# Optimization experiments

Measured on AMD Instinct MI355X. Metric: run time of the kernel, lower is better.

The kernel has to match this reference:

```python
import jax, jax.numpy as jnp
import numpy as np

TEMPERATURE = 0.2
NUMBER_CLASSES = 1000
LOSS_SCALE = 0.001

N, F = 8192, 256
M = 20000
DEPTH = 4


def setup_inputs() -> dict:
    key = jax.random.key(0)
    k1, k2, k3, k4 = jax.random.split(key, 4)
    gt_labels = jax.random.randint(k1, (N,), 0, NUMBER_CLASSES, dtype=jnp.int32)
    box_features = jax.random.normal(k2, (N, F), dtype=jnp.float32)
    memory = jax.random.normal(k3, (M, F), dtype=jnp.float32)
    trace_idx = jax.random.randint(k4, (NUMBER_CLASSES, DEPTH), 0, M, dtype=jnp.int32)
    return {"gt_labels": gt_labels, "box_features": box_features,
            "memory": memory, "trace_idx": trace_idx}


def reference(gt_labels, box_features, memory, trace_idx):
    # logits[i, j] = dot(f_i, m_j) / T  (the nested python loops fused into one GEMM)
    logits = jnp.einsum('nf,mf->nm', box_features, memory) / TEMPERATURE  # [N, M]
    # fenmu = sum_j exp(logits)  ->  log(fenmu) = logsumexp
    lse = jax.nn.logsumexp(logits, axis=-1)  # [N]
    # gather the trace entries for each item's label: [N, DEPTH]
    traces = trace_idx[gt_labels]  # [N, DEPTH]
    sel = jnp.take_along_axis(logits, traces, axis=1)  # [N, DEPTH]
    depth_w = jnp.arange(DEPTH, dtype=logits.dtype)  # gj = depth
    sum_gj = depth_w.sum()  # sum of layer weights (0+1+2+3)
    # per item: -sum_d gj * log(sim_d / fenmu) / sum_gj
    per_item = -jnp.sum((sel - lse[:, None]) * depth_w, axis=-1) / sum_gj  # [N]
    # background filter: items with label == number_classes contribute nothing
    fg = (gt_labels != NUMBER_CLASSES)
    loss = jnp.sum(jnp.where(fg, per_item, 0.0)) * LOSS_SCALE
    return loss
```

## Files before the change

### kernel.cpp

```cpp
#include <hip/hip_runtime.h>
#include <hip/hip_bf16.h>
#include <stdint.h>

#define NROWS 8192
#define FDIM 256
#define MCOLS 20000
#define NT32 625
#define MSPLIT 16
#define NCLS 1000
#define LOG2E 1.44269504088896f
#define LN2   0.69314718055994f


typedef short short8 __attribute__((ext_vector_type(8)));
typedef float f32x16 __attribute__((ext_vector_type(16)));

typedef __attribute__((address_space(3))) unsigned int lds_u32;
typedef const __attribute__((address_space(1))) unsigned int glb_u32;

__device__ __forceinline__ float ex2(float x) {
    float r;
    asm("v_exp_f32 %0, %1" : "=v"(r) : "v"(x));
    return r;
}

__device__ __forceinline__ unsigned short f2bf(float x) {
    unsigned u = __float_as_uint(x);
    unsigned r = (u + 0x7FFFu + ((u >> 16) & 1u)) >> 16;
    return (unsigned short)r;
}

__device__ __forceinline__ float vmax16(f32x16 v) {
    float x0 = fmaxf(fmaxf(v[0],  v[1]),  v[2]);
    float x1 = fmaxf(fmaxf(v[3],  v[4]),  v[5]);
    float x2 = fmaxf(fmaxf(v[6],  v[7]),  v[8]);
    float x3 = fmaxf(fmaxf(v[9],  v[10]), v[11]);
    float x4 = fmaxf(fmaxf(v[12], v[13]), v[14]);
    float x5 = fmaxf(fmaxf(x0, x1), x2);
    float x6 = fmaxf(fmaxf(x3, x4), v[15]);
    return fmaxf(x5, x6);
}

__global__ void conv_kernel(const float* __restrict__ in, unsigned short* __restrict__ out,
                            int n4, float scale) {
    int idx = blockIdx.x * blockDim.x + threadIdx.x;
    if (idx >= n4) return;
    float4 v = ((const float4*)in)[idx];
    ushort4 o;
    o.x = f2bf(v.x * scale); o.y = f2bf(v.y * scale);
    o.z = f2bf(v.z * scale); o.w = f2bf(v.w * scale);
    ((ushort4*)out)[idx] = o;
}

__global__ void conv_mb2(const float* __restrict__ in, unsigned short* __restrict__ out) {
    int g = blockIdx.x * 256 + threadIdx.x;
    int s = g & 63, kk = (g >> 6) & 15, t = g >> 10;
    const float* src = in + (size_t)(t * 32 + (s & 31)) * FDIM + kk * 16 + (s >> 5) * 8;
    float4 v0 = ((const float4*)src)[0];
    float4 v1 = ((const float4*)src)[1];
    short8 w;
    w[0] = (short)f2bf(v0.x); w[1] = (short)f2bf(v0.y);
    w[2] = (short)f2bf(v0.z); w[3] = (short)f2bf(v0.w);
    w[4] = (short)f2bf(v1.x); w[5] = (short)f2bf(v1.y);
    w[6] = (short)f2bf(v1.z); w[7] = (short)f2bf(v1.w);
    *(short8*)(out + (size_t)g * 8) = w;
}

__global__ void sel_kernel(const int* __restrict__ gt, const float* __restrict__ F,
                           const float* __restrict__ Mem, const int* __restrict__ trace,
                           float* __restrict__ wsel) {
    int lane = threadIdx.x & 63, wid = threadIdx.x >> 6;
    int i = blockIdx.x * 4 + wid;
    int label = gt[i];
    float w = 0.0f;
    if (label >= 0 && label < NCLS) {
        float4 fv = ((const float4*)(F + (size_t)i * FDIM))[lane];
        #pragma unroll
        for (int d = 1; d <= 3; ++d) {
            int tr = trace[label * 4 + d];
            float4 mv = ((const float4*)(Mem + (size_t)tr * FDIM))[lane];
            float dot = fv.x*mv.x + fv.y*mv.y + fv.z*mv.z + fv.w*mv.w;
            #pragma unroll
            for (int off = 32; off >= 1; off >>= 1) dot += __shfl_xor(dot, off, 64);
            w += (float)d * dot;
        }
    }
    if (lane == 0) wsel[i] = w * 5.0f;
}

__global__ __launch_bounds__(256, 2) void lse_gemm(
        const unsigned short* __restrict__ Fb, const unsigned short* __restrict__ Mb2,
        float* __restrict__ pm, float* __restrict__ ps) {
    __shared__ __align__(16) char smem[2 * 16384];

    const int split  = blockIdx.x;
    const int rowblk = blockIdx.y;
    const int tid  = threadIdx.x;
    const int lane = tid & 63, wid = tid >> 6;
    const int r0 = lane & 31;
    const int hi = lane >> 5;
    const int rowbase = rowblk * 256 + wid * 64;
    const int l16 = lane << 4;

    short8 al[16], ah[16];
    #pragma unroll
    for (int kk = 0; kk < 16; ++kk) {
        al[kk] = *(const short8*)(Fb + (size_t)(rowbase + r0)      * FDIM + kk * 16 + hi * 8);
        ah[kk] = *(const short8*)(Fb + (size_t)(rowbase + 32 + r0) * FDIM + kk * 16 + hi * 8);
    }

    float m0 = -3.0e38f, s0 = 0.0f, m1 = -3.0e38f, s1 = 0.0f;

    const int t0 = (split * NT32) / MSPLIT;
    const int t1 = ((split + 1) * NT32) / MSPLIT;

#define STAGE(BUF, t)                                                              \
    do {                                                                           \
        const char* srcT = (const char*)Mb2 + (size_t)(t) * 16384 + l16;           \
        _Pragma("unroll")                                                          \
        for (int c = 0; c < 4; ++c) {                                              \
            __builtin_amdgcn_global_load_lds(                                      \
                (glb_u32*)(srcT + (wid * 4 + c) * 1024),                           \
                (lds_u32*)(smem + (BUF) * 16384 + (wid * 4 + c) * 1024),           \
                16, 0, 0);                                                         \
        }                                                                          \
    } while (0)

#define BODYC(BUF)                                                                 \
    do {                                                                           \
        const char* bp = smem + (BUF) * 16384 + l16;                               \
        f32x16 accL = {0,0,0,0,0,0,0,0,0,0,0,0,0,0,0,0};                           \
        f32x16 accH = {0,0,0,0,0,0,0,0,0,0,0,0,0,0,0,0};                           \
        __builtin_amdgcn_s_setprio(1);                                             \
        _Pragma("unroll")                                                          \
        for (int kk = 0; kk < 16; ++kk) {                                          \
            short8 b = *(const short8*)(bp + kk * 1024);                           \
            accL = __builtin_amdgcn_mfma_f32_32x32x16_bf16(b, al[kk], accL, 0, 0, 0); \
            accH = __builtin_amdgcn_mfma_f32_32x32x16_bf16(b, ah[kk], accH, 0, 0, 0); \
        }                                                                          \
        __builtin_amdgcn_s_setprio(0);                                             \
        {                                                                          \
            float nm = fmaxf(vmax16(accL), m0);                                    \
            float p0 = 0.f, p1 = 0.f, p2 = 0.f, p3 = 0.f;                          \
            _Pragma("unroll")                                                      \
            for (int i = 0; i < 16; i += 4) {                                      \
                p0 += ex2(accL[i]     - nm); p1 += ex2(accL[i + 1] - nm);          \
                p2 += ex2(accL[i + 2] - nm); p3 += ex2(accL[i + 3] - nm);          \
            }                                                                      \
            s0 = fmaf(s0, ex2(m0 - nm), (p0 + p1) + (p2 + p3));                    \
            m0 = nm;                                                               \
        }                                                                          \
        {                                                                          \
            float nm = fmaxf(vmax16(accH), m1);                                    \
            float p0 = 0.f, p1 = 0.f, p2 = 0.f, p3 = 0.f;                          \
            _Pragma("unroll")                                                      \
            for (int i = 0; i < 16; i += 4) {                                      \
                p0 += ex2(accH[i]     - nm); p1 += ex2(accH[i + 1] - nm);          \
                p2 += ex2(accH[i + 2] - nm); p3 += ex2(accH[i + 3] - nm);          \
            }                                                                      \
            s1 = fmaf(s1, ex2(m1 - nm), (p0 + p1) + (p2 + p3));                    \
            m1 = nm;                                                               \
        }                                                                          \
    } while (0)

    STAGE(0, t0);
    __syncthreads();

    int t = t0;
    while (t + 2 <= t1) {
        STAGE(1, t + 1);
        BODYC(0);
        __syncthreads();
        if (t + 2 < t1) STAGE(0, t + 2);
        BODYC(1);
        __syncthreads();
        t += 2;
    }
    if (t < t1) BODYC(0);

#undef BODYC
#undef STAGE

    {
        float om = __shfl_xor(m0, 32, 64);
        float os = __shfl_xor(s0, 32, 64);
        float nm = fmaxf(m0, om);
        float sf = fmaf(s0, ex2(m0 - nm), os * ex2(om - nm));
        if (lane < 32) {
            pm[split * NROWS + rowbase + lane] = nm;
            ps[split * NROWS + rowbase + lane] = sf;
        }
    }
    {
        float om = __shfl_xor(m1, 32, 64);
        float os = __shfl_xor(s1, 32, 64);
        float nm = fmaxf(m1, om);
        float sf = fmaf(s1, ex2(m1 - nm), os * ex2(om - nm));
        if (lane < 32) {
            pm[split * NROWS + rowbase + 32 + lane] = nm;
            ps[split * NROWS + rowbase + 32 + lane] = sf;
        }
    }
}

__global__ void finalize_kernel(const int* __restrict__ gt, const float* __restrict__ wsel,
                                const float* __restrict__ pm, const float* __restrict__ ps,
                                float* __restrict__ bpart) {
    int tid = threadIdx.x;
    int i = blockIdx.x * 256 + tid;
    float mv[MSPLIT];
    float M = -3.0e38f;
    #pragma unroll
    for (int k = 0; k < MSPLIT; ++k) { mv[k] = pm[k * NROWS + i]; M = fmaxf(M, mv[k]); }
    float S = 0.0f;
    #pragma unroll
    for (int k = 0; k < MSPLIT; ++k) S += ps[k * NROWS + i] * ex2(mv[k] - M);
    float lse = (M + __log2f(S)) * LN2;
    int label = gt[i];
    float per = (label >= 0 && label < NCLS) ? (lse - wsel[i] * (1.0f / 6.0f)) : 0.0f;
    #pragma unroll
    for (int off = 32; off >= 1; off >>= 1) per += __shfl_xor(per, off, 64);
    __shared__ float red[4];
    int lane = tid & 63, wid = tid >> 6;
    if (lane == 0) red[wid] = per;
    __syncthreads();
    if (tid == 0) bpart[blockIdx.x] = red[0] + red[1] + red[2] + red[3];
}

__global__ void sum_kernel(const float* __restrict__ bpart, float* __restrict__ out) {
    int tid = threadIdx.x;
    float v = (tid < 32) ? bpart[tid] : 0.0f;
    #pragma unroll
    for (int off = 32; off >= 1; off >>= 1) v += __shfl_xor(v, off, 64);
    if (tid == 0) out[0] = 0.001f * v;
}

extern "C" void kernel_launch(void* const* d_in, const int* in_sizes, int n_in,
                              void* d_out, int out_size, void* d_ws, size_t ws_size,
                              hipStream_t stream) {
    const int*   gt    = (const int*)d_in[0];
    const float* F     = (const float*)d_in[1];
    const float* Mem   = (const float*)d_in[2];
    const int*   trace = (const int*)d_in[3];
    float* out = (float*)d_out;

    char* w = (char*)d_ws;
    unsigned short* Mb2 = (unsigned short*)w;
    unsigned short* Fb  = (unsigned short*)(w + 10240000);
    float* wsel  = (float*)(w + 14434304);
    float* pm    = (float*)(w + 14467072);
    float* ps    = (float*)(w + 14991360);
    float* bpart = (float*)(w + 15515648);

    conv_mb2<<<dim3(2500), dim3(256), 0, stream>>>(Mem, Mb2);
    conv_kernel<<<dim3((NROWS * FDIM / 4) / 256), dim3(256), 0, stream>>>(F, Fb, NROWS * FDIM / 4, 5.0f * LOG2E);
    sel_kernel<<<dim3(NROWS / 4), dim3(256), 0, stream>>>(gt, F, Mem, trace, wsel);
    lse_gemm<<<dim3(MSPLIT, NROWS / 256), dim3(256), 0, stream>>>(Fb, Mb2, pm, ps);
    finalize_kernel<<<dim3(NROWS / 256), dim3(256), 0, stream>>>(gt, wsel, pm, ps, bpart);
    sum_kernel<<<dim3(1), dim3(64), 0, stream>>>(bpart, out);
}
```

Measured before the change: 102.4 us.

## Stage two memory tiles per barrier and merge conversion kernels

```diff
diff --git a/kernel.cpp b/kernel.cpp
--- a/kernel.cpp
+++ b/kernel.cpp
@@ -41,29 +41,30 @@
     return fmaxf(x5, x6);
 }
 
-__global__ void conv_kernel(const float* __restrict__ in, unsigned short* __restrict__ out,
-                            int n4, float scale) {
-    int idx = blockIdx.x * blockDim.x + threadIdx.x;
-    if (idx >= n4) return;
-    float4 v = ((const float4*)in)[idx];
-    ushort4 o;
-    o.x = f2bf(v.x * scale); o.y = f2bf(v.y * scale);
-    o.z = f2bf(v.z * scale); o.w = f2bf(v.w * scale);
-    ((ushort4*)out)[idx] = o;
-}
-
-__global__ void conv_mb2(const float* __restrict__ in, unsigned short* __restrict__ out) {
-    int g = blockIdx.x * 256 + threadIdx.x;
-    int s = g & 63, kk = (g >> 6) & 15, t = g >> 10;
-    const float* src = in + (size_t)(t * 32 + (s & 31)) * FDIM + kk * 16 + (s >> 5) * 8;
-    float4 v0 = ((const float4*)src)[0];
-    float4 v1 = ((const float4*)src)[1];
-    short8 w;
-    w[0] = (short)f2bf(v0.x); w[1] = (short)f2bf(v0.y);
-    w[2] = (short)f2bf(v0.z); w[3] = (short)f2bf(v0.w);
-    w[4] = (short)f2bf(v1.x); w[5] = (short)f2bf(v1.y);
-    w[6] = (short)f2bf(v1.z); w[7] = (short)f2bf(v1.w);
-    *(short8*)(out + (size_t)g * 8) = w;
+__global__ void prep_kernel(const float* __restrict__ Mem, unsigned short* __restrict__ Mb2,
+                            const float* __restrict__ F, unsigned short* __restrict__ Fb) {
+    int b = blockIdx.x;
+    if (b < 2500) {
+        int g = b * 256 + threadIdx.x;
+        int s = g & 63, kk = (g >> 6) & 15, t = g >> 10;
+        const float* src = Mem + (size_t)(t * 32 + (s & 31)) * FDIM + kk * 16 + (s >> 5) * 8;
+        float4 v0 = ((const float4*)src)[0];
+        float4 v1 = ((const float4*)src)[1];
+        short8 w;
+        w[0] = (short)f2bf(v0.x); w[1] = (short)f2bf(v0.y);
+        w[2] = (short)f2bf(v0.z); w[3] = (short)f2bf(v0.w);
+        w[4] = (short)f2bf(v1.x); w[5] = (short)f2bf(v1.y);
+        w[6] = (short)f2bf(v1.z); w[7] = (short)f2bf(v1.w);
+        *(short8*)(Mb2 + (size_t)g * 8) = w;
+    } else {
+        int idx = (b - 2500) * 256 + threadIdx.x;
+        float4 v = ((const float4*)F)[idx];
+        const float sc = 5.0f * LOG2E;
+        ushort4 o;
+        o.x = f2bf(v.x * sc); o.y = f2bf(v.y * sc);
+        o.z = f2bf(v.z * sc); o.w = f2bf(v.w * sc);
+        ((ushort4*)Fb)[idx] = o;
+    }
 }
 
 __global__ void sel_kernel(const int* __restrict__ gt, const float* __restrict__ F,
@@ -91,7 +92,7 @@
 __global__ __launch_bounds__(256, 2) void lse_gemm(
         const unsigned short* __restrict__ Fb, const unsigned short* __restrict__ Mb2,
         float* __restrict__ pm, float* __restrict__ ps) {
-    __shared__ __align__(16) char smem[2 * 16384];
+    __shared__ __align__(16) char smem[2 * 32768];
 
     const int split  = blockIdx.x;
     const int rowblk = blockIdx.y;
@@ -113,22 +114,35 @@
 
     const int t0 = (split * NT32) / MSPLIT;
     const int t1 = ((split + 1) * NT32) / MSPLIT;
-
-#define STAGE(BUF, t)                                                              \
+    const int nt = t1 - t0, nmac = nt >> 1, tail = nt & 1;
+
+#define STAGE2(BUF, t)                                                             \
+    do {                                                                           \
+        const char* srcT = (const char*)Mb2 + (size_t)(t) * 16384 + l16;           \
+        _Pragma("unroll")                                                          \
+        for (int c = 0; c < 8; ++c) {                                              \
+            __builtin_amdgcn_global_load_lds(                                      \
+                (glb_u32*)(srcT + (wid * 8 + c) * 1024),                           \
+                (lds_u32*)(smem + (BUF) * 32768 + (wid * 8 + c) * 1024),           \
+                16, 0, 0);                                                         \
+        }                                                                          \
+    } while (0)
+
+#define STAGE1(BUF, t)                                                             \
     do {                                                                           \
         const char* srcT = (const char*)Mb2 + (size_t)(t) * 16384 + l16;           \
         _Pragma("unroll")                                                          \
         for (int c = 0; c < 4; ++c) {                                              \
             __builtin_amdgcn_global_load_lds(                                      \
                 (glb_u32*)(srcT + (wid * 4 + c) * 1024),                           \
-                (lds_u32*)(smem + (BUF) * 16384 + (wid * 4 + c) * 1024),           \
+                (lds_u32*)(smem + (BUF) * 32768 + (wid * 4 + c) * 1024),           \
                 16, 0, 0);                                                         \
         }                                                                          \
     } while (0)
 
-#define BODYC(BUF)                                                                 \
+#define SUB(BB)                                                                    \
     do {                                                                           \
-        const char* bp = smem + (BUF) * 16384 + l16;                               \
+        const char* bp = smem + (BB) + l16;                                        \
         f32x16 accL = {0,0,0,0,0,0,0,0,0,0,0,0,0,0,0,0};                           \
         f32x16 accH = {0,0,0,0,0,0,0,0,0,0,0,0,0,0,0,0};                           \
         __builtin_amdgcn_s_setprio(1);                                             \
@@ -163,23 +177,22 @@
         }                                                                          \
     } while (0)
 
-    STAGE(0, t0);
+    STAGE2(0, t0);
     __syncthreads();
 
-    int t = t0;
-    while (t + 2 <= t1) {
-        STAGE(1, t + 1);
-        BODYC(0);
+    for (int mi = 0; mi < nmac; ++mi) {
+        const int bb = (mi & 1) * 32768;
+        if (mi + 1 < nmac)      STAGE2((mi & 1) ^ 1, t0 + 2 * mi + 2);
+        else if (tail)          STAGE1((mi & 1) ^ 1, t0 + 2 * mi + 2);
+        SUB(bb);
+        SUB(bb + 16384);
         __syncthreads();
-        if (t + 2 < t1) STAGE(0, t + 2);
-        BODYC(1);
-        __syncthreads();
-        t += 2;
-    }
-    if (t < t1) BODYC(0);
-
-#undef BODYC
-#undef STAGE
+    }
+    if (tail) SUB((nmac & 1) * 32768);
+
+#undef SUB
+#undef STAGE1
+#undef STAGE2
 
     {
         float om = __shfl_xor(m0, 32, 64);
@@ -252,8 +265,7 @@
     float* ps    = (float*)(w + 14991360);
     float* bpart = (float*)(w + 15515648);
 
-    conv_mb2<<<dim3(2500), dim3(256), 0, stream>>>(Mem, Mb2);
-    conv_kernel<<<dim3((NROWS * FDIM / 4) / 256), dim3(256), 0, stream>>>(F, Fb, NROWS * FDIM / 4, 5.0f * LOG2E);
+    prep_kernel<<<dim3(4548), dim3(256), 0, stream>>>(Mem, Mb2, F, Fb);
     sel_kernel<<<dim3(NROWS / 4), dim3(256), 0, stream>>>(gt, F, Mem, trace, wsel);
     lse_gemm<<<dim3(MSPLIT, NROWS / 256), dim3(256), 0, stream>>>(Fb, Mb2, pm, ps);
     finalize_kernel<<<dim3(NROWS / 256), dim3(256), 0, stream>>>(gt, wsel, pm, ps, bpart);
```

Measured after the change: 103.3 us. Within noise of the previous version (+0.9%).
